# Optimization experiments

Measured on AMD Instinct MI355X. Metric: run time of the kernel, lower is better.

Reference implementation:

```python
import jax, jax.numpy as jnp
import numpy as np

NUM_HOPS = 3
NUM_GRAPHS = 2048
N_NODES = 50000
N_EDGES = 2400000
HIDDEN = 128
EMB = 64
N_LAYERS = 3
N_MLP = 2
N_HEADS = 4


def setup_inputs() -> dict:
    key = jax.random.key(0)
    ks = iter(jax.random.split(key, 64))
    nk = lambda: next(ks)
    f = lambda shape: jax.random.normal(nk(), shape, dtype=jnp.float32) * 0.05
    inp = {}
    inp["atom_type"] = jax.random.randint(nk(), (N_NODES,), 0, 100)
    inp["hydrogen_count"] = jax.random.randint(nk(), (N_NODES,), 0, 9)
    inp["degree"] = jax.random.randint(nk(), (N_NODES,), 0, 8)
    inp["hybridization"] = jax.random.randint(nk(), (N_NODES,), 0, 8)
    inp["target"] = jax.random.randint(nk(), (N_EDGES,), 0, NUM_HOPS * N_NODES)
    inp["src"] = jax.random.randint(nk(), (N_EDGES,), 0, NUM_HOPS * N_NODES)
    inp["batch_indices"] = jnp.sort(jax.random.randint(nk(), (N_NODES,), 0, NUM_GRAPHS))
    # learned parameters
    inp["emb_atom"] = f((100, EMB))
    inp["emb_h"] = f((9, EMB))
    inp["emb_deg"] = f((8, EMB))
    inp["emb_hyb"] = f((8, EMB))
    inp["proj_w"] = f((4 * EMB, HIDDEN)); inp["proj_b"] = jnp.zeros((HIDDEN,), jnp.float32)
    IN = HIDDEN * (NUM_HOPS + 1)
    inp["shell_in_w"] = f((N_LAYERS, IN, HIDDEN)); inp["shell_in_b"] = jnp.zeros((N_LAYERS, HIDDEN), jnp.float32)
    inp["shell_mlp_w1"] = f((N_LAYERS, N_MLP, HIDDEN, HIDDEN)); inp["shell_mlp_b1"] = jnp.zeros((N_LAYERS, N_MLP, HIDDEN), jnp.float32)
    inp["shell_mlp_w2"] = f((N_LAYERS, N_MLP, HIDDEN, HIDDEN)); inp["shell_mlp_b2"] = jnp.zeros((N_LAYERS, N_MLP, HIDDEN), jnp.float32)
    inp["shell_skip_w"] = f((N_LAYERS, IN, HIDDEN)); inp["shell_skip_b"] = jnp.zeros((N_LAYERS, HIDDEN), jnp.float32)
    inp["attn_w"] = f((N_HEADS, HIDDEN)); inp["attn_b"] = jnp.zeros((N_HEADS,), jnp.float32)
    inp["temperature"] = jnp.array(1.0, jnp.float32)
    inp["ffn_w1"] = f((HIDDEN, HIDDEN)); inp["ffn_b1"] = jnp.zeros((HIDDEN,), jnp.float32)
    inp["ffn_w2"] = f((HIDDEN, HIDDEN)); inp["ffn_b2"] = jnp.zeros((HIDDEN,), jnp.float32)
    inp["ffn_w3"] = f((HIDDEN, 1)); inp["ffn_b3"] = jnp.zeros((1,), jnp.float32)
    return inp


def _forward(atom_type, hydrogen_count, degree, hybridization, target, src, batch_indices,
             emb_atom, emb_h, emb_deg, emb_hyb, proj_w, proj_b,
             shell_in_w, shell_in_b, shell_mlp_w1, shell_mlp_b1, shell_mlp_w2, shell_mlp_b2,
             shell_skip_w, shell_skip_b, attn_w, attn_b, temperature,
             ffn_w1, ffn_b1, ffn_w2, ffn_b2, ffn_w3, ffn_b3):
    act = jax.nn.silu
    n = atom_type.shape[0]
    # atom embedding: concat of 4 lookups -> projection (dropout off / eval mode)
    emb = jnp.concatenate([emb_atom[atom_type], emb_h[hydrogen_count],
                           emb_deg[degree], emb_hyb[hybridization]], axis=-1)  # [N, 4*EMB]
    x = act(emb @ proj_w + proj_b)  # [N, H]
    for l in range(N_LAYERS):
        # shell convolution: hop aggregation via gather + index_add over expanded [hops*N, H]
        expanded = jnp.tile(x, (NUM_HOPS, 1))                              # [hops*N, H]
        agg = jnp.zeros_like(expanded).at[target].add(expanded[src])
        hops = agg.reshape(NUM_HOPS, n, HIDDEN)                            # split into hop chunks
        feats = jnp.concatenate([x[None], hops], axis=0)                   # [hops+1, N, H]
        feats = jnp.moveaxis(feats, 0, 1).reshape(n, (NUM_HOPS + 1) * HIDDEN)  # cat([x, hop0..], -1)
        h = act(feats @ shell_in_w[l] + shell_in_b[l])
        gskip = feats @ shell_skip_w[l] + shell_skip_b[l]
        for m in range(N_MLP):
            skip = h
            h = act(h @ shell_mlp_w1[l, m] + shell_mlp_b1[l, m])
            h = h @ shell_mlp_w2[l, m] + shell_mlp_b2[l, m]
            h = h + skip
        x = h + gskip
    # multi-head attention pooling with scatter-softmax over graphs
    scores = (x @ attn_w.T + attn_b) / temperature                         # [N, heads]
    smax = jax.ops.segment_max(scores, batch_indices, num_segments=NUM_GRAPHS)
    ex = jnp.exp(scores - smax[batch_indices])
    denom = jax.ops.segment_sum(ex, batch_indices, num_segments=NUM_GRAPHS)
    w = ex / denom[batch_indices]                                          # [N, heads]
    weighted = (x[:, None, :] * w[:, :, None]).reshape(n, N_HEADS * HIDDEN)
    pooled = jax.ops.segment_sum(weighted, batch_indices, num_segments=NUM_GRAPHS)
    pooled = pooled.reshape(NUM_GRAPHS, N_HEADS, HIDDEN).mean(axis=1)      # mean over heads
    # FFN readout
    h = act(pooled @ ffn_w1 + ffn_b1)
    h = act(h @ ffn_w2 + ffn_b2)
    return h @ ffn_w3 + ffn_b3                                             # [G, 1]


def reference(atom_type, hydrogen_count, degree, hybridization, target, src, batch_indices,
              emb_atom, emb_h, emb_deg, emb_hyb, proj_w, proj_b,
              shell_in_w, shell_in_b, shell_mlp_w1, shell_mlp_b1, shell_mlp_w2, shell_mlp_b2,
              shell_skip_w, shell_skip_b, attn_w, attn_b, temperature,
              ffn_w1, ffn_b1, ffn_w2, ffn_b2, ffn_w3, ffn_b3):
    return _forward(atom_type, hydrogen_count, degree, hybridization, target, src, batch_indices,
                    emb_atom, emb_h, emb_deg, emb_hyb, proj_w, proj_b,
                    shell_in_w, shell_in_b, shell_mlp_w1, shell_mlp_b1, shell_mlp_w2, shell_mlp_b2,
                    shell_skip_w, shell_skip_b, attn_w, attn_b, temperature,
                    ffn_w1, ffn_b1, ffn_w2, ffn_b2, ffn_w3, ffn_b3)
```

## Files before the change

### kernel.cpp

```cpp
#include <hip/hip_runtime.h>
#include <math.h>

#define NN      50000
#define NNP     50048
#define NE      2400000
#define NHOPS   3
#define NG      2048
#define H       128
#define EMBD    64
#define NL      3
#define NMLP    2
#define NHEADS  4
#define NROWS   (NHOPS * NN)
#define BINSH   9
#define NBIN    293
#define CAPB    10240
#define ABLK    480
#define DEPTH   32
#define LSTR    136
#define SENT    0xFFFFFFFFu

typedef __bf16 bf16x8 __attribute__((ext_vector_type(8)));
typedef __bf16 bf16x4 __attribute__((ext_vector_type(4)));
typedef float  f32x4  __attribute__((ext_vector_type(4)));

__device__ __forceinline__ float silu_f(float v) { return v / (1.0f + expf(-v)); }

__device__ __forceinline__ f32x4 mm(bf16x8 a, bf16x8 b, f32x4 c) {
    return __builtin_amdgcn_mfma_f32_16x16x32_bf16(a, b, c, 0, 0, 0);
}

__device__ __forceinline__ float blo(unsigned v) { return __builtin_bit_cast(float, v << 16); }
__device__ __forceinline__ float bhi(unsigned v) { return __builtin_bit_cast(float, v & 0xffff0000u); }
__device__ __forceinline__ unsigned pk2(float a, float b) {
    unsigned short ua = __builtin_bit_cast(unsigned short, (__bf16)a);
    unsigned short ub = __builtin_bit_cast(unsigned short, (__bf16)b);
    return (unsigned)ua | ((unsigned)ub << 16);
}

__device__ __forceinline__ void packw_elem(
    const float* __restrict__ W, __bf16* __restrict__ out, int K, long idx)
{
    long per = (long)K * 128;
    long mat = idx / per, e = idx - mat * per;
    int j = (int)(e & 7), n16 = (int)((e >> 3) & 15), q = (int)((e >> 7) & 3),
        mt = (int)((e >> 9) & 7), kt = (int)(e >> 12);
    int k = kt * 32 + q * 8 + j, n = mt * 16 + n16;
    out[idx] = (__bf16)W[mat * per + (long)k * 128 + n];
}

__global__ __launch_bounds__(256) void k_packall(
    const float* __restrict__ projW, __bf16* __restrict__ pproj,
    const float* __restrict__ sInW,  __bf16* __restrict__ pin,
    const float* __restrict__ sSkW,  __bf16* __restrict__ psk,
    const float* __restrict__ mW1,   __bf16* __restrict__ pw1,
    const float* __restrict__ mW2,   __bf16* __restrict__ pw2,
    const float* __restrict__ Ea, const float* __restrict__ Eh,
    const float* __restrict__ Ed, const float* __restrict__ Ey,
    __bf16* __restrict__ embb)
{
    long tid = (long)blockIdx.x * 256 + threadIdx.x;
    if (tid < 32768) { packw_elem(projW, pproj, 256, tid); return; }
    tid -= 32768;
    if (tid < 196608) { packw_elem(sInW, pin, 512, tid); return; }
    tid -= 196608;
    if (tid < 196608) { packw_elem(sSkW, psk, 512, tid); return; }
    tid -= 196608;
    if (tid < 98304) { packw_elem(mW1, pw1, 128, tid); return; }
    tid -= 98304;
    if (tid < 98304) { packw_elem(mW2, pw2, 128, tid); return; }
    tid -= 98304;
    if (tid < 8000) {
        int t = (int)tid;
        float v;
        if (t < 6400) v = Ea[t];
        else if (t < 6976) v = Eh[t - 6400];
        else if (t < 7488) v = Ed[t - 6976];
        else v = Ey[t - 7488];
        embb[t] = (__bf16)v;
    }
}

__global__ __launch_bounds__(256) void k_embed_m(
    const int* __restrict__ atom, const int* __restrict__ hc,
    const int* __restrict__ deg,  const int* __restrict__ hyb,
    const __bf16* __restrict__ emb, const __bf16* __restrict__ pw,
    const float* __restrict__ pb, __bf16* __restrict__ x)
{
    const int lane = threadIdx.x & 63, wid = threadIdx.x >> 6;
    const int q = lane >> 4, l16 = lane & 15;
    const int nb = blockIdx.x * 128 + wid * 32;
    int ia[2][4];
#pragma unroll
    for (int nt = 0; nt < 2; ++nt) {
        int n = nb + nt * 16 + l16;
        if (n >= NN) n = NN - 1;
        ia[nt][0] = atom[n]; ia[nt][1] = hc[n]; ia[nt][2] = deg[n]; ia[nt][3] = hyb[n];
    }
    f32x4 acc[2][8];
#pragma unroll
    for (int nt = 0; nt < 2; ++nt)
#pragma unroll
        for (int mt = 0; mt < 8; ++mt) acc[nt][mt] = (f32x4)(0.f);
    const int tb[4] = {0, 6400, 6976, 7488};
    for (int kt = 0; kt < 8; ++kt) {
        int t = kt >> 1;
        int koff = (kt & 1) * 32 + q * 8;
        bf16x8 bfrag[2];
#pragma unroll
        for (int nt = 0; nt < 2; ++nt)
            bfrag[nt] = *(const bf16x8*)(emb + tb[t] + (long)ia[nt][t] * 64 + koff);
        const __bf16* ap = pw + (long)kt * 4096 + lane * 8;
#pragma unroll
        for (int mt = 0; mt < 8; ++mt) {
            bf16x8 a = *(const bf16x8*)(ap + mt * 512);
            acc[0][mt] = mm(a, bfrag[0], acc[0][mt]);
            acc[1][mt] = mm(a, bfrag[1], acc[1][mt]);
        }
    }
#pragma unroll
    for (int nt = 0; nt < 2; ++nt) {
        long node = nb + nt * 16 + l16;
#pragma unroll
        for (int mt = 0; mt < 8; ++mt) {
            int ch = mt * 16 + q * 4;
            float4 bb = *(const float4*)(pb + ch);
            bf16x4 o;
            o[0] = (__bf16)silu_f(acc[nt][mt][0] + bb.x);
            o[1] = (__bf16)silu_f(acc[nt][mt][1] + bb.y);
            o[2] = (__bf16)silu_f(acc[nt][mt][2] + bb.z);
            o[3] = (__bf16)silu_f(acc[nt][mt][3] + bb.w);
            *(bf16x4*)(x + node * 128 + ch) = o;
        }
    }
}

__global__ __launch_bounds__(256) void k_binA(
    const int* __restrict__ target, const int* __restrict__ src,
    int* __restrict__ gbincur, int* __restrict__ brealc,
    unsigned int* __restrict__ binreg)
{
    __shared__ unsigned int buf[NBIN][DEPTH];
    __shared__ int cnt[NBIN];
    __shared__ int flushed[NBIN];
    const int tid = threadIdx.x;
    for (int i = tid; i < NBIN; i += 256) { cnt[i] = 0; flushed[i] = 0; }
    __syncthreads();
    const int per = (NE + ABLK - 1) / ABLK;
    const int e0 = blockIdx.x * per;
    const int e1 = (e0 + per < NE) ? e0 + per : NE;
    for (int base = e0; base < e1; base += 256) {
        int e = base + tid;
        if (e < e1) {
            int s = src[e];
            if (s >= 2 * NN) s -= 2 * NN; else if (s >= NN) s -= NN;
            int t = target[e];
            int bin = t >> BINSH;
            unsigned val = (unsigned)s | ((unsigned)(t & ((1 << BINSH) - 1)) << 16);
            int slot = atomicAdd(&cnt[bin], 1);
            buf[bin][slot & (DEPTH - 1)] = val;
        }
        __syncthreads();
        for (int b = tid; b < NBIN; b += 256) {
            while (cnt[b] - flushed[b] >= 16) {
                int pos = atomicAdd(&gbincur[b], 16);
                if (pos + 16 <= CAPB) {
                    uint4* d4 = (uint4*)(binreg + (long)b * CAPB + pos);
                    const uint4* s4 = (const uint4*)&buf[b][flushed[b] & (DEPTH - 1)];
                    d4[0] = s4[0]; d4[1] = s4[1]; d4[2] = s4[2]; d4[3] = s4[3];
                }
                flushed[b] += 16;
            }
        }
        __syncthreads();
    }
    for (int b = tid; b < NBIN; b += 256) {
        int lvl = cnt[b] - flushed[b];
        if (cnt[b] > 0) atomicAdd(&brealc[b], cnt[b]);
        if (lvl > 0) {
            int pad = (lvl + 3) & ~3;
            int pos = atomicAdd(&gbincur[b], pad);
            for (int i = 0; i < pad; i += 4) {
                uint4 v;
                v.x = (i + 0 < lvl) ? buf[b][(flushed[b] + i + 0) & (DEPTH - 1)] : SENT;
                v.y = (i + 1 < lvl) ? buf[b][(flushed[b] + i + 1) & (DEPTH - 1)] : SENT;
                v.z = (i + 2 < lvl) ? buf[b][(flushed[b] + i + 2) & (DEPTH - 1)] : SENT;
                v.w = (i + 3 < lvl) ? buf[b][(flushed[b] + i + 3) & (DEPTH - 1)] : SENT;
                if (pos + i + 4 <= CAPB)
                    *(uint4*)(binreg + (long)b * CAPB + pos + i) = v;
            }
        }
    }
}

__global__ __launch_bounds__(512) void k_fill2b(
    const unsigned int* __restrict__ binreg, const int* __restrict__ gbincur,
    const int* __restrict__ brealc, int* __restrict__ csr_start,
    unsigned short* __restrict__ esrc)
{
    __shared__ unsigned int stage[CAPB];
    __shared__ int pc[512], rcnt[512], scn[512], cur[512];
    const int b = blockIdx.x, tid = threadIdx.x;
    int pv = (tid < NBIN) ? brealc[tid] : 0;
    if (pv < 0) pv = 0;
    pc[tid] = pv;
    __syncthreads();
    for (int off = 1; off < 512; off <<= 1) {
        int t = (tid >= off) ? pc[tid - off] : 0;
        __syncthreads();
        pc[tid] += t;
        __syncthreads();
    }
    int bbase = (b == 0) ? 0 : pc[b - 1];
    int total = gbincur[b];
    if (total > CAPB) total = CAPB;
    if (total < 0) total = 0;
    const unsigned int* seg = binreg + (long)b * CAPB;
    for (int i = tid; i < total; i += 512) stage[i] = seg[i];
    rcnt[tid] = 0;
    __syncthreads();
    for (int i = tid; i < total; i += 512) {
        unsigned pk = stage[i];
        if (pk != SENT) atomicAdd(&rcnt[(pk >> 16) & 511], 1);
    }
    __syncthreads();
    int v = rcnt[tid];
    scn[tid] = v;
    __syncthreads();
    for (int off = 1; off < 512; off <<= 1) {
        int t = (tid >= off) ? scn[tid - off] : 0;
        __syncthreads();
        scn[tid] += t;
        __syncthreads();
    }
    int base = bbase + scn[tid] - v;
    cur[tid] = base;
    int row = b * 512 + tid;
    if (row <= NROWS) csr_start[row] = base;
    __syncthreads();
    for (int i = tid; i < total; i += 512) {
        unsigned pk = stage[i];
        if (pk != SENT) {
            int pos = atomicAdd(&cur[(pk >> 16) & 511], 1);
            if (pos >= 0 && pos < NE) esrc[pos] = (unsigned short)(pk & 0xffffu);
        }
    }
}

__global__ __launch_bounds__(256) void k_gather(
    const unsigned short* __restrict__ esrc, const int* __restrict__ csr_start,
    const uint4* __restrict__ x8, uint4* __restrict__ agg8)
{
    int row = blockIdx.x * 16 + (threadIdx.x >> 4);
    int lane = threadIdx.x & 63;
    int l4 = lane & 15, qw = lane >> 4;
    int e0 = csr_start[row], e1 = csr_start[row + 1];
    if ((unsigned)e0 > NE || (unsigned)e1 > NE || e1 < e0) { e0 = 0; e1 = 0; }
    int nch = (e1 - e0 + 15) >> 4;
    int n0 = __shfl(nch, 0, 64), n1 = __shfl(nch, 16, 64);
    int n2 = __shfl(nch, 32, 64), n3 = __shfl(nch, 48, 64);
    int nmax = max(max(n0, n1), max(n2, n3));
    float a0 = 0.f, a1 = 0.f, a2 = 0.f, a3 = 0.f, a4 = 0.f, a5 = 0.f, a6 = 0.f, a7 = 0.f;
    const int sb = qw << 4;
    for (int c = 0; c < nmax; ++c) {
        int base = e0 + c * 16;
        int rem = e1 - base;
        int pre = (l4 < rem) ? (int)esrc[base + l4] : 0;
        int m = rem < 16 ? (rem < 0 ? 0 : rem) : 16;
        int j = 0;
        for (; j + 3 < m; j += 4) {
            int sA = __shfl(pre, sb + j, 64);
            int sB = __shfl(pre, sb + j + 1, 64);
            int sC = __shfl(pre, sb + j + 2, 64);
            int sD = __shfl(pre, sb + j + 3, 64);
            uint4 v0 = x8[(long)sA * 16 + l4];
            uint4 v1 = x8[(long)sB * 16 + l4];
            uint4 v2 = x8[(long)sC * 16 + l4];
            uint4 v3 = x8[(long)sD * 16 + l4];
            a0 += blo(v0.x) + blo(v1.x) + blo(v2.x) + blo(v3.x);
            a1 += bhi(v0.x) + bhi(v1.x) + bhi(v2.x) + bhi(v3.x);
            a2 += blo(v0.y) + blo(v1.y) + blo(v2.y) + blo(v3.y);
            a3 += bhi(v0.y) + bhi(v1.y) + bhi(v2.y) + bhi(v3.y);
            a4 += blo(v0.z) + blo(v1.z) + blo(v2.z) + blo(v3.z);
            a5 += bhi(v0.z) + bhi(v1.z) + bhi(v2.z) + bhi(v3.z);
            a6 += blo(v0.w) + blo(v1.w) + blo(v2.w) + blo(v3.w);
            a7 += bhi(v0.w) + bhi(v1.w) + bhi(v2.w) + bhi(v3.w);
        }
        for (; j < m; ++j) {
            int sA = __shfl(pre, sb + j, 64);
            uint4 v0 = x8[(long)sA * 16 + l4];
            a0 += blo(v0.x); a1 += bhi(v0.x); a2 += blo(v0.y); a3 += bhi(v0.y);
            a4 += blo(v0.z); a5 += bhi(v0.z); a6 += blo(v0.w); a7 += bhi(v0.w);
        }
    }
    int hop = row / NN, node = row - hop * NN;
    uint4 o;
    o.x = pk2(a0, a1); o.y = pk2(a2, a3); o.z = pk2(a4, a5); o.w = pk2(a6, a7);
    agg8[((long)hop * NNP + node) * 16 + l4] = o;
}

__global__ __launch_bounds__(256) void k_layer(
    const __bf16* __restrict__ x, const __bf16* __restrict__ agg,
    const __bf16* __restrict__ pwin, const float* __restrict__ bin,
    const __bf16* __restrict__ pwsk, const float* __restrict__ bsk,
    const __bf16* __restrict__ pw1a, const float* __restrict__ b1a,
    const __bf16* __restrict__ pw2a, const float* __restrict__ b2a,
    const __bf16* __restrict__ pw1b, const float* __restrict__ b1b,
    const __bf16* __restrict__ pw2b, const float* __restrict__ b2b,
    __bf16* __restrict__ xout)
{
    __shared__ __bf16 lds[2][16 * LSTR];
    const int lane = threadIdx.x & 63, wid = threadIdx.x >> 6;
    const int pair = wid >> 1, half = wid & 1;
    const int q = lane >> 4, l16 = lane & 15;
    const int nb = blockIdx.x * 32 + pair * 16;
    const int mtoff = half * 4 * 512;
    const int chb = half * 64;
    const int la = lane * 8;
    __bf16* L = lds[pair];
    const long r0 = (long)(nb + l16) * 128;
    const __bf16* planes[4] = {x, agg, agg + (long)NNP * 128, agg + 2L * NNP * 128};

    bf16x8 ring[8];
#pragma unroll
    for (int k = 0; k < 8; ++k)
        ring[k] = *(const bf16x8*)(planes[k >> 2] + (k & 3) * 32 + q * 8 + r0);
    f32x4 aci[4], acs[4];
#pragma unroll
    for (int mt = 0; mt < 4; ++mt) { aci[mt] = (f32x4)(0.f); acs[mt] = (f32x4)(0.f); }
#pragma unroll
    for (int kt = 0; kt < 16; ++kt) {
        bf16x8 b0 = ring[kt & 7];
        if (kt < 8) {
            int k2 = kt + 8;
            ring[kt & 7] = *(const bf16x8*)(planes[k2 >> 2] + (k2 & 3) * 32 + q * 8 + r0);
        }
        const __bf16* aip = pwin + (long)kt * 4096 + mtoff + la;
        const __bf16* asp = pwsk + (long)kt * 4096 + mtoff + la;
#pragma unroll
        for (int mt = 0; mt < 4; ++mt) {
            aci[mt] = mm(*(const bf16x8*)(aip + mt * 512), b0, aci[mt]);
            acs[mt] = mm(*(const bf16x8*)(asp + mt * 512), b0, acs[mt]);
        }
    }
    bf16x4 gk[4];
    bf16x4 hs[4];
#pragma unroll
    for (int mt = 0; mt < 4; ++mt) {
        int ch = chb + mt * 16 + q * 4;
        float4 bi = *(const float4*)(bin + ch);
        float4 bs = *(const float4*)(bsk + ch);
        bf16x4 oh, og;
        oh[0] = (__bf16)silu_f(aci[mt][0] + bi.x);
        oh[1] = (__bf16)silu_f(aci[mt][1] + bi.y);
        oh[2] = (__bf16)silu_f(aci[mt][2] + bi.z);
        oh[3] = (__bf16)silu_f(aci[mt][3] + bi.w);
        og[0] = (__bf16)(acs[mt][0] + bs.x);
        og[1] = (__bf16)(acs[mt][1] + bs.y);
        og[2] = (__bf16)(acs[mt][2] + bs.z);
        og[3] = (__bf16)(acs[mt][3] + bs.w);
        hs[mt] = oh; gk[mt] = og;
        *(bf16x4*)(L + l16 * LSTR + ch) = oh;
    }
    __syncthreads();

    f32x4 acc[4];
    bf16x4 skipreg[4];

#pragma unroll
    for (int mt = 0; mt < 4; ++mt) acc[mt] = (f32x4)(0.f);
#pragma unroll
    for (int kt = 0; kt < 4; ++kt) {
        int koff = kt * 32 + q * 8;
        bf16x8 f0 = *(const bf16x8*)(L + l16 * LSTR + koff);
        const __bf16* ap = pw1a + (long)kt * 4096 + mtoff + la;
#pragma unroll
        for (int mt = 0; mt < 4; ++mt)
            acc[mt] = mm(*(const bf16x8*)(ap + mt * 512), f0, acc[mt]);
    }
    __syncthreads();
#pragma unroll
    for (int mt = 0; mt < 4; ++mt) {
        int ch = chb + mt * 16 + q * 4;
        float4 bb = *(const float4*)(b1a + ch);
        bf16x4 o;
        o[0] = (__bf16)silu_f(acc[mt][0] + bb.x);
        o[1] = (__bf16)silu_f(acc[mt][1] + bb.y);
        o[2] = (__bf16)silu_f(acc[mt][2] + bb.z);
        o[3] = (__bf16)silu_f(acc[mt][3] + bb.w);
        *(bf16x4*)(L + l16 * LSTR + ch) = o;
    }
    __syncthreads();

#pragma unroll
    for (int mt = 0; mt < 4; ++mt) acc[mt] = (f32x4)(0.f);
#pragma unroll
    for (int kt = 0; kt < 4; ++kt) {
        int koff = kt * 32 + q * 8;
        bf16x8 f0 = *(const bf16x8*)(L + l16 * LSTR + koff);
        const __bf16* ap = pw2a + (long)kt * 4096 + mtoff + la;
#pragma unroll
        for (int mt = 0; mt < 4; ++mt)
            acc[mt] = mm(*(const bf16x8*)(ap + mt * 512), f0, acc[mt]);
    }
    __syncthreads();
#pragma unroll
    for (int mt = 0; mt < 4; ++mt) {
        int ch = chb + mt * 16 + q * 4;
        float4 bb = *(const float4*)(b2a + ch);
        bf16x4 sk = hs[mt];
        bf16x4 o;
        o[0] = (__bf16)(acc[mt][0] + bb.x + (float)sk[0]);
        o[1] = (__bf16)(acc[mt][1] + bb.y + (float)sk[1]);
        o[2] = (__bf16)(acc[mt][2] + bb.z + (float)sk[2]);
        o[3] = (__bf16)(acc[mt][3] + bb.w + (float)sk[3]);
        skipreg[mt] = o;
        *(bf16x4*)(L + l16 * LSTR + ch) = o;
    }
    __syncthreads();

#pragma unroll
    for (int mt = 0; mt < 4; ++mt) acc[mt] = (f32x4)(0.f);
#pragma unroll
    for (int kt = 0; kt < 4; ++kt) {
        int koff = kt * 32 + q * 8;
        bf16x8 f0 = *(const bf16x8*)(L + l16 * LSTR + koff);
        const __bf16* ap = pw1b + (long)kt * 4096 + mtoff + la;
#pragma unroll
        for (int mt = 0; mt < 4; ++mt)
            acc[mt] = mm(*(const bf16x8*)(ap + mt * 512), f0, acc[mt]);
    }
    __syncthreads();
#pragma unroll
    for (int mt = 0; mt < 4; ++mt) {
        int ch = chb + mt * 16 + q * 4;
        float4 bb = *(const float4*)(b1b + ch);
        bf16x4 o;
        o[0] = (__bf16)silu_f(acc[mt][0] + bb.x);
        o[1] = (__bf16)silu_f(acc[mt][1] + bb.y);
        o[2] = (__bf16)silu_f(acc[mt][2] + bb.z);
        o[3] = (__bf16)silu_f(acc[mt][3] + bb.w);
        *(bf16x4*)(L + l16 * LSTR + ch) = o;
    }
    __syncthreads();

#pragma unroll
    for (int mt = 0; mt < 4; ++mt) acc[mt] = (f32x4)(0.f);
#pragma unroll
    for (int kt = 0; kt < 4; ++kt) {
        int koff = kt * 32 + q * 8;
        bf16x8 f0 = *(const bf16x8*)(L + l16 * LSTR + koff);
        const __bf16* ap = pw2b + (long)kt * 4096 + mtoff + la;
#pragma unroll
        for (int mt = 0; mt < 4; ++mt)
            acc[mt] = mm(*(const bf16x8*)(ap + mt * 512), f0, acc[mt]);
    }
    long node = nb + l16;
#pragma unroll
    for (int mt = 0; mt < 4; ++mt) {
        int ch = chb + mt * 16 + q * 4;
        float4 bb = *(const float4*)(b2b + ch);
        bf16x4 sk = skipreg[mt];
        bf16x4 g = gk[mt];
        bf16x4 o;
        o[0] = (__bf16)(acc[mt][0] + bb.x + (float)sk[0] + (float)g[0]);
        o[1] = (__bf16)(acc[mt][1] + bb.y + (float)sk[1] + (float)g[1]);
        o[2] = (__bf16)(acc[mt][2] + bb.z + (float)sk[2] + (float)g[2]);
        o[3] = (__bf16)(acc[mt][3] + bb.w + (float)sk[3] + (float)g[3]);
        *(bf16x4*)(xout + node * 128 + ch) = o;
    }
}

__global__ __launch_bounds__(256) void k_scores(
    const __bf16* __restrict__ x, const float* __restrict__ aw,
    const float* __restrict__ ab, const float* __restrict__ temp,
    float* __restrict__ scores)
{
    int wave = threadIdx.x >> 6, lane = threadIdx.x & 63;
    int n = blockIdx.x * 4 + wave;
    if (n >= NN) return;
    float x0 = (float)x[(long)n * H + lane];
    float x1 = (float)x[(long)n * H + 64 + lane];
    float T = temp[0];
#pragma unroll
    for (int hh = 0; hh < NHEADS; ++hh) {
        float p = x0 * aw[hh * H + lane] + x1 * aw[hh * H + 64 + lane];
#pragma unroll
        for (int off = 32; off >= 1; off >>= 1) p += __shfl_xor(p, off, 64);
        if (lane == 0) scores[n * NHEADS + hh] = (p + ab[hh]) / T;
    }
}

__global__ __launch_bounds__(256) void k_offsets(
    const int* __restrict__ batch, int* __restrict__ gstart)
{
    int n = blockIdx.x * 256 + threadIdx.x;
    if (n >= NN) return;
    int b = batch[n];
    int bp = (n == 0) ? -1 : batch[n - 1];
    for (int g = bp + 1; g <= b; ++g) gstart[g] = n;
    if (n == NN - 1) for (int g = b + 1; g <= NG; ++g) gstart[g] = NN;
}

__global__ __launch_bounds__(64) void k_pool(
    const __bf16* __restrict__ x, const float* __restrict__ scores,
    const int* __restrict__ gstart, float* __restrict__ pooled)
{
    int g = blockIdx.x, lane = threadIdx.x;
    int s0 = gstart[g], s1 = gstart[g + 1];
    float m0 = -INFINITY, m1 = -INFINITY, m2 = -INFINITY, m3 = -INFINITY;
    for (int n = s0 + lane; n < s1; n += 64) {
        m0 = fmaxf(m0, scores[n * 4 + 0]); m1 = fmaxf(m1, scores[n * 4 + 1]);
        m2 = fmaxf(m2, scores[n * 4 + 2]); m3 = fmaxf(m3, scores[n * 4 + 3]);
    }
#pragma unroll
    for (int off = 32; off >= 1; off >>= 1) {
        m0 = fmaxf(m0, __shfl_xor(m0, off, 64)); m1 = fmaxf(m1, __shfl_xor(m1, off, 64));
        m2 = fmaxf(m2, __shfl_xor(m2, off, 64)); m3 = fmaxf(m3, __shfl_xor(m3, off, 64));
    }
    float d0 = 0.f, d1 = 0.f, d2 = 0.f, d3 = 0.f;
    for (int n = s0 + lane; n < s1; n += 64) {
        d0 += expf(scores[n * 4 + 0] - m0); d1 += expf(scores[n * 4 + 1] - m1);
        d2 += expf(scores[n * 4 + 2] - m2); d3 += expf(scores[n * 4 + 3] - m3);
    }
#pragma unroll
    for (int off = 32; off >= 1; off >>= 1) {
        d0 += __shfl_xor(d0, off, 64); d1 += __shfl_xor(d1, off, 64);
        d2 += __shfl_xor(d2, off, 64); d3 += __shfl_xor(d3, off, 64);
    }
    float i0 = d0 > 0.f ? 1.f / d0 : 0.f;
    float i1 = d1 > 0.f ? 1.f / d1 : 0.f;
    float i2 = d2 > 0.f ? 1.f / d2 : 0.f;
    float i3 = d3 > 0.f ? 1.f / d3 : 0.f;
    float a0 = 0.f, a1 = 0.f;
    for (int n = s0; n < s1; ++n) {
        float wb = expf(scores[n * 4 + 0] - m0) * i0 + expf(scores[n * 4 + 1] - m1) * i1
                 + expf(scores[n * 4 + 2] - m2) * i2 + expf(scores[n * 4 + 3] - m3) * i3;
        wb *= 0.25f;
        a0 += wb * (float)x[(long)n * H + lane];
        a1 += wb * (float)x[(long)n * H + 64 + lane];
    }
    pooled[g * H + lane] = a0;
    pooled[g * H + 64 + lane] = a1;
}

__global__ __launch_bounds__(128) void k_ffn(
    const float* __restrict__ pooled,
    const float* __restrict__ W1, const float* __restrict__ B1,
    const float* __restrict__ W2, const float* __restrict__ B2,
    const float* __restrict__ W3, const float* __restrict__ B3,
    float* __restrict__ out)
{
    __shared__ float p[H], t1[H], t2[H], red[H];
    int g = blockIdx.x, c = threadIdx.x;
    p[c] = pooled[g * H + c];
    __syncthreads();
    float acc = 0.f;
    for (int k = 0; k < H; ++k) acc += p[k] * W1[k * H + c];
    t1[c] = silu_f(acc + B1[c]);
    __syncthreads();
    acc = 0.f;
    for (int k = 0; k < H; ++k) acc += t1[k] * W2[k * H + c];
    t2[c] = silu_f(acc + B2[c]);
    __syncthreads();
    red[c] = t2[c] * W3[c];
    __syncthreads();
    for (int off = 64; off >= 1; off >>= 1) {
        if (c < off) red[c] += red[c + off];
        __syncthreads();
    }
    if (c == 0) out[g] = red[0] + B3[0];
}

extern "C" void kernel_launch(void* const* d_in, const int* in_sizes, int n_in,
                              void* d_out, int out_size, void* d_ws, size_t ws_size,
                              hipStream_t stream)
{
    const int*   atom   = (const int*)d_in[0];
    const int*   hc     = (const int*)d_in[1];
    const int*   deg    = (const int*)d_in[2];
    const int*   hyb    = (const int*)d_in[3];
    const int*   target = (const int*)d_in[4];
    const int*   src    = (const int*)d_in[5];
    const int*   batch  = (const int*)d_in[6];
    const float* Ea     = (const float*)d_in[7];
    const float* Eh     = (const float*)d_in[8];
    const float* Ed     = (const float*)d_in[9];
    const float* Ey     = (const float*)d_in[10];
    const float* projW  = (const float*)d_in[11];
    const float* projB  = (const float*)d_in[12];
    const float* sInW   = (const float*)d_in[13];
    const float* sInB   = (const float*)d_in[14];
    const float* mW1    = (const float*)d_in[15];
    const float* mB1    = (const float*)d_in[16];
    const float* mW2    = (const float*)d_in[17];
    const float* mB2    = (const float*)d_in[18];
    const float* sSkW   = (const float*)d_in[19];
    const float* sSkB   = (const float*)d_in[20];
    const float* attnW  = (const float*)d_in[21];
    const float* attnB  = (const float*)d_in[22];
    const float* temp   = (const float*)d_in[23];
    const float* fW1    = (const float*)d_in[24];
    const float* fB1    = (const float*)d_in[25];
    const float* fW2    = (const float*)d_in[26];
    const float* fB2    = (const float*)d_in[27];
    const float* fW3    = (const float*)d_in[28];
    const float* fB3    = (const float*)d_in[29];
    float* out = (float*)d_out;

    char* w = (char*)d_ws;
    auto take = [&](size_t bytes) { void* p = (void*)w; w += (bytes + 255) & ~(size_t)255; return p; };
    __bf16* x      = (__bf16*)take(2L * NNP * H);
    __bf16* agg    = (__bf16*)take(2L * 3 * NNP * H);
    __bf16* pproj  = (__bf16*)take(2L * 256 * H);
    __bf16* pin    = (__bf16*)take(2L * 3 * 512 * H);
    __bf16* psk    = (__bf16*)take(2L * 3 * 512 * H);
    __bf16* pw1    = (__bf16*)take(2L * 6 * 128 * H);
    __bf16* pw2    = (__bf16*)take(2L * 6 * 128 * H);
    __bf16* embb   = (__bf16*)take(2L * 8000);
    float*  scores = (float*)take(4L * NN * NHEADS);
    float*  pooled = (float*)take(4L * NG * H);
    int*    gstart = (int*)take(4L * (NG + 1));
    int*    csr_start = (int*)take(4L * (NROWS + 1));
    unsigned int*   binreg = (unsigned int*)take(4L * NBIN * CAPB);
    unsigned short* esrc   = (unsigned short*)take(2L * NE);
    int*    gbincur = (int*)take(4L * 2 * NBIN);
    int*    brealc  = gbincur + NBIN;

    k_packall<<<(630592 + 255) / 256, 256, 0, stream>>>(
        projW, pproj, sInW, pin, sSkW, psk, mW1, pw1, mW2, pw2,
        Ea, Eh, Ed, Ey, embb);

    hipMemsetAsync(gbincur, 0, sizeof(int) * 2 * NBIN, stream);
    k_binA<<<ABLK, 256, 0, stream>>>(target, src, gbincur, brealc, binreg);
    k_fill2b<<<NBIN, 512, 0, stream>>>(binreg, gbincur, brealc, csr_start, esrc);

    k_embed_m<<<NNP / 128, 256, 0, stream>>>(atom, hc, deg, hyb, embb, pproj, projB, x);
    k_offsets<<<(NN + 255) / 256, 256, 0, stream>>>(batch, gstart);

    for (int l = 0; l < NL; ++l) {
        k_gather<<<NROWS / 16, 256, 0, stream>>>(esrc, csr_start,
            (const uint4*)x, (uint4*)agg);
        k_layer<<<NNP / 32, 256, 0, stream>>>(x, agg,
            pin + (long)l * 512 * H, sInB + l * H,
            psk + (long)l * 512 * H, sSkB + l * H,
            pw1 + (long)(l * NMLP + 0) * 128 * H, mB1 + (long)(l * NMLP + 0) * H,
            pw2 + (long)(l * NMLP + 0) * 128 * H, mB2 + (long)(l * NMLP + 0) * H,
            pw1 + (long)(l * NMLP + 1) * 128 * H, mB1 + (long)(l * NMLP + 1) * H,
            pw2 + (long)(l * NMLP + 1) * 128 * H, mB2 + (long)(l * NMLP + 1) * H,
            x);
    }

    k_scores<<<NN / 4, 256, 0, stream>>>(x, attnW, attnB, temp, scores);
    k_pool<<<NG, 64, 0, stream>>>(x, scores, gstart, pooled);
    k_ffn<<<NG, 128, 0, stream>>>(pooled, fW1, fB1, fW2, fB2, fW3, fB3, out);
}
```

Baseline: 696.8 us.

## Split CSR fill per bin into two half-blocks and shrink layer blocks

Each CSR bin is now filled by two blocks, each owning half of the bin's 512 target rows. Each block filters and stages only its own edges in LDS and computes its base offset from the bin total minus its own count. The binning kernel gets more blocks and a larger per-bin capacity. The layer kernel now runs 128-thread blocks over 16 nodes instead of 256-thread blocks over 32, which gives more, smaller blocks for scheduling. Each half-block rereads the whole bin segment from global memory, and a bin holding more than STG edges for one half would be truncated.

```diff
diff --git a/kernel.cpp b/kernel.cpp
--- a/kernel.cpp
+++ b/kernel.cpp
@@ -14,9 +14,10 @@
 #define NROWS   (NHOPS * NN)
 #define BINSH   9
 #define NBIN    293
-#define CAPB    10240
-#define ABLK    480
+#define CAPB    12288
+#define ABLK    1024
 #define DEPTH   32
+#define STG     6144
 #define LSTR    136
 #define SENT    0xFFFFFFFFu
 
@@ -198,12 +199,17 @@
     const int* __restrict__ brealc, int* __restrict__ csr_start,
     unsigned short* __restrict__ esrc)
 {
-    __shared__ unsigned int stage[CAPB];
-    __shared__ int pc[512], rcnt[512], scn[512], cur[512];
-    const int b = blockIdx.x, tid = threadIdx.x;
+    __shared__ unsigned int stage[STG];
+    __shared__ int pc[512], rcnt[256], scn[256], cur[256];
+    __shared__ int nstage;
+    const int blk = blockIdx.x;
+    const int b = blk >> 1, half = blk & 1;
+    const int tid = threadIdx.x;
     int pv = (tid < NBIN) ? brealc[tid] : 0;
     if (pv < 0) pv = 0;
     pc[tid] = pv;
+    if (tid == 0) nstage = 0;
+    if (tid < 256) rcnt[tid] = 0;
     __syncthreads();
     for (int off = 1; off < 512; off <<= 1) {
         int t = (tid >= off) ? pc[tid - off] : 0;
@@ -211,39 +217,45 @@
         pc[tid] += t;
         __syncthreads();
     }
-    int bbase = (b == 0) ? 0 : pc[b - 1];
+    const int bbase = (b == 0) ? 0 : pc[b - 1];
+    const int breal = pc[b] - bbase;
     int total = gbincur[b];
     if (total > CAPB) total = CAPB;
     if (total < 0) total = 0;
     const unsigned int* seg = binreg + (long)b * CAPB;
-    for (int i = tid; i < total; i += 512) stage[i] = seg[i];
-    rcnt[tid] = 0;
-    __syncthreads();
     for (int i = tid; i < total; i += 512) {
+        unsigned pk = seg[i];
+        if (pk == SENT) continue;
+        int tl = (pk >> 16) & 511;
+        if ((tl >> 8) == half) {
+            int p = atomicAdd(&nstage, 1);
+            if (p < STG) stage[p] = pk;
+            atomicAdd(&rcnt[tl & 255], 1);
+        }
+    }
+    __syncthreads();
+    int own = nstage; if (own > STG) own = STG;
+    const int base0 = bbase + (half ? (breal - own) : 0);
+    if (tid < 256) scn[tid] = rcnt[tid];
+    __syncthreads();
+    for (int off = 1; off < 256; off <<= 1) {
+        int t = (tid >= off && tid < 256) ? scn[tid - off] : 0;
+        __syncthreads();
+        if (tid < 256) scn[tid] += t;
+        __syncthreads();
+    }
+    if (tid < 256) {
+        int v = rcnt[tid];
+        int rb = base0 + scn[tid] - v;
+        cur[tid] = rb;
+        int row = b * 512 + half * 256 + tid;
+        if (row <= NROWS) csr_start[row] = rb;
+    }
+    __syncthreads();
+    for (int i = tid; i < own; i += 512) {
         unsigned pk = stage[i];
-        if (pk != SENT) atomicAdd(&rcnt[(pk >> 16) & 511], 1);
-    }
-    __syncthreads();
-    int v = rcnt[tid];
-    scn[tid] = v;
-    __syncthreads();
-    for (int off = 1; off < 512; off <<= 1) {
-        int t = (tid >= off) ? scn[tid - off] : 0;
-        __syncthreads();
-        scn[tid] += t;
-        __syncthreads();
-    }
-    int base = bbase + scn[tid] - v;
-    cur[tid] = base;
-    int row = b * 512 + tid;
-    if (row <= NROWS) csr_start[row] = base;
-    __syncthreads();
-    for (int i = tid; i < total; i += 512) {
-        unsigned pk = stage[i];
-        if (pk != SENT) {
-            int pos = atomicAdd(&cur[(pk >> 16) & 511], 1);
-            if (pos >= 0 && pos < NE) esrc[pos] = (unsigned short)(pk & 0xffffu);
-        }
+        int pos = atomicAdd(&cur[(pk >> 16) & 255], 1);
+        if (pos >= 0 && pos < NE) esrc[pos] = (unsigned short)(pk & 0xffffu);
     }
 }
 
@@ -299,7 +311,7 @@
     agg8[((long)hop * NNP + node) * 16 + l4] = o;
 }
 
-__global__ __launch_bounds__(256) void k_layer(
+__global__ __launch_bounds__(128) void k_layer(
     const __bf16* __restrict__ x, const __bf16* __restrict__ agg,
     const __bf16* __restrict__ pwin, const float* __restrict__ bin,
     const __bf16* __restrict__ pwsk, const float* __restrict__ bsk,
@@ -309,15 +321,13 @@
     const __bf16* __restrict__ pw2b, const float* __restrict__ b2b,
     __bf16* __restrict__ xout)
 {
-    __shared__ __bf16 lds[2][16 * LSTR];
-    const int lane = threadIdx.x & 63, wid = threadIdx.x >> 6;
-    const int pair = wid >> 1, half = wid & 1;
+    __shared__ __bf16 L[16 * LSTR];
+    const int lane = threadIdx.x & 63, half = threadIdx.x >> 6;
     const int q = lane >> 4, l16 = lane & 15;
-    const int nb = blockIdx.x * 32 + pair * 16;
+    const int nb = blockIdx.x * 16;
     const int mtoff = half * 4 * 512;
     const int chb = half * 64;
     const int la = lane * 8;
-    __bf16* L = lds[pair];
     const long r0 = (long)(nb + l16) * 128;
     const __bf16* planes[4] = {x, agg, agg + (long)NNP * 128, agg + 2L * NNP * 128};
 
@@ -633,7 +643,7 @@
 
     hipMemsetAsync(gbincur, 0, sizeof(int) * 2 * NBIN, stream);
     k_binA<<<ABLK, 256, 0, stream>>>(target, src, gbincur, brealc, binreg);
-    k_fill2b<<<NBIN, 512, 0, stream>>>(binreg, gbincur, brealc, csr_start, esrc);
+    k_fill2b<<<2 * NBIN, 512, 0, stream>>>(binreg, gbincur, brealc, csr_start, esrc);
 
     k_embed_m<<<NNP / 128, 256, 0, stream>>>(atom, hc, deg, hyb, embb, pproj, projB, x);
     k_offsets<<<(NN + 255) / 256, 256, 0, stream>>>(batch, gstart);
@@ -641,7 +651,7 @@
     for (int l = 0; l < NL; ++l) {
         k_gather<<<NROWS / 16, 256, 0, stream>>>(esrc, csr_start,
             (const uint4*)x, (uint4*)agg);
-        k_layer<<<NNP / 32, 256, 0, stream>>>(x, agg,
+        k_layer<<<NNP / 16, 128, 0, stream>>>(x, agg,
             pin + (long)l * 512 * H, sInB + l * H,
             psk + (long)l * 512 * H, sSkB + l * H,
             pw1 + (long)(l * NMLP + 0) * 128 * H, mB1 + (long)(l * NMLP + 0) * H,
```

New measurement: 657.9 us, median of 2. 1.06x faster.
